# Kernel tuning notes

Measured on AMD Instinct MI355X. Metric: run time of the kernel, lower is better.

The kernel has to match this reference:

```python
import jax, jax.numpy as jnp
import numpy as np

# Mamba2 defaults: d_model=256, d_state=64, d_conv=4, expand=2, headdim=64, ngroups=1
D_MODEL = 256
NB = 2            # num_blocks
D_STATE = 64
D_CONV = 4
D_INNER = 2 * D_MODEL          # 512
HEADDIM = 64
NHEADS = D_INNER // HEADDIM    # 8
CONV_DIM = D_INNER + 2 * D_STATE           # 640
D_IN_PROJ = 2 * D_INNER + 2 * D_STATE + NHEADS  # 1160
EPS = 1e-5


def setup_inputs() -> dict:
    key = jax.random.key(0)
    ks = jax.random.split(key, 10)
    x = jax.random.normal(ks[0], (8, 32, 32, D_MODEL), dtype=jnp.float32)
    in_proj_w = jax.random.normal(ks[1], (NB, D_IN_PROJ, D_MODEL), dtype=jnp.float32) * 0.02
    conv_w = jax.random.normal(ks[2], (NB, CONV_DIM, 1, D_CONV), dtype=jnp.float32) * 0.2
    conv_b = jax.random.normal(ks[3], (NB, CONV_DIM), dtype=jnp.float32) * 0.02
    dt_bias = jax.random.normal(ks[4], (NB, NHEADS), dtype=jnp.float32) * 0.5
    # A_log = log(A), A ~ U[1,16) as in mamba2 init
    A_log = jnp.log(jax.random.uniform(ks[5], (NB, NHEADS), minval=1.0, maxval=16.0, dtype=jnp.float32))
    D = jax.random.normal(ks[6], (NB, NHEADS), dtype=jnp.float32) * 0.1 + 1.0
    norm_w = jnp.ones((NB, D_INNER), dtype=jnp.float32)
    out_proj_w = jax.random.normal(ks[7], (NB, D_MODEL, D_INNER), dtype=jnp.float32) * 0.02
    return {"x": x, "in_proj_w": in_proj_w, "conv_w": conv_w, "conv_b": conv_b,
            "dt_bias": dt_bias, "A_log": A_log, "D": D, "norm_w": norm_w,
            "out_proj_w": out_proj_w}


def _mamba2_block(h, wi, cw, cb, dtb, a_log, d_skip, nw, wo):
    B, L, _ = h.shape
    zxbcdt = jnp.einsum('blc,pc->blp', h, wi)                 # (B,L,1160)
    z = zxbcdt[..., :D_INNER]                                 # (B,L,512)
    xBC = zxbcdt[..., D_INNER:D_INNER + CONV_DIM]             # (B,L,640)
    dt = jax.nn.softplus(zxbcdt[..., -NHEADS:] + dtb)         # (B,L,8)

    # causal depthwise conv1d, kernel 4, left pad 3
    xBC = jax.lax.conv_general_dilated(
        xBC.swapaxes(1, 2), cw, window_strides=(1,), padding=[(D_CONV - 1, 0)],
        dimension_numbers=('NCH', 'OIH', 'NCH'), feature_group_count=CONV_DIM)
    xBC = jax.nn.silu((xBC + cb[None, :, None]).swapaxes(1, 2))  # (B,L,640)

    xs = xBC[..., :D_INNER].reshape(B, L, NHEADS, HEADDIM)    # (B,L,h,p)
    Bm = xBC[..., D_INNER:D_INNER + D_STATE]                  # (B,L,s) ngroups=1
    Cm = xBC[..., D_INNER + D_STATE:]                         # (B,L,s)

    A = -jnp.exp(a_log)                                       # (h,)
    dA = jnp.exp(dt * A)                                      # (B,L,h)

    def step(s, inp):
        dA_t, dt_t, x_t, B_t, C_t = inp  # (B,h),(B,h),(B,h,p),(B,s),(B,s)
        s = s * dA_t[:, :, None, None] + (dt_t[:, :, None] * x_t)[..., None] * B_t[:, None, None, :]
        y = jnp.einsum('bhps,bs->bhp', s, C_t)
        return s, y

    s0 = jnp.zeros((B, NHEADS, HEADDIM, D_STATE), dtype=h.dtype)
    _, ys = jax.lax.scan(step, s0, (dA.swapaxes(0, 1), dt.swapaxes(0, 1),
                                    xs.swapaxes(0, 1), Bm.swapaxes(0, 1), Cm.swapaxes(0, 1)))
    y = ys.swapaxes(0, 1) + d_skip[:, None] * xs              # (B,L,h,p)
    y = y.reshape(B, L, D_INNER) * jax.nn.silu(z)             # gate
    y = y * jax.lax.rsqrt(jnp.mean(y * y, axis=-1, keepdims=True) + EPS) * nw  # gated RMSNorm
    return jnp.einsum('bld,cd->blc', y, wo)


def reference(x, in_proj_w, conv_w, conv_b, dt_bias, A_log, D, norm_w, out_proj_w):
    B, H, W, C = x.shape
    h = x.reshape(B, H * W, C)
    for i in range(NB):  # stacked blocks; Dropout is identity at inference
        h = _mamba2_block(h, in_proj_w[i], conv_w[i], conv_b[i], dt_bias[i],
                          A_log[i], D[i], norm_w[i], out_proj_w[i])
    return h.reshape(B, H, W, C)
```

## Files before the change

### kernel.cpp

```cpp
#include <hip/hip_runtime.h>
#include <hip/hip_bf16.h>
#include <math.h>

#define D_MODEL   256
#define D_STATE   64
#define D_CONV    4
#define D_INNER   512
#define HEADDIM   64
#define NHEADS    8
#define CONV_DIM  640
#define D_IN_PROJ 1160
#define ZXP       1280
#define SEQLEN    1024
#define BATCH     8
#define NROWS     8192
#define EPS       1e-5f
#define CHUNK     64
#define NCHUNK    (SEQLEN / CHUNK)

typedef __attribute__((ext_vector_type(8))) short bf16x8;
typedef __attribute__((ext_vector_type(4))) short s16x4;
typedef __attribute__((ext_vector_type(8))) unsigned short u16x8;
typedef __attribute__((ext_vector_type(4))) unsigned short u16x4;
typedef __attribute__((ext_vector_type(4))) float f32x4;
typedef unsigned int u32;
typedef unsigned short u16;

__device__ __forceinline__ void cp16(const short* g, short* l) {
    __builtin_amdgcn_global_load_lds((const __attribute__((address_space(1))) u32*)g,
                                     (__attribute__((address_space(3))) u32*)l, 16, 0, 0);
}
__device__ __forceinline__ u16 bfc(float f) {
    union { __hip_bfloat16 h; u16 u; } cv;
    cv.h = __float2bfloat16(f);
    return cv.u;
}
__device__ __forceinline__ float bf2f(u16 u) {
    union { u32 v; float f; } cv;
    cv.v = ((u32)u) << 16;
    return cv.f;
}
__device__ __forceinline__ float silu_f(float a) {
    return a * __builtin_amdgcn_rcpf(1.f + __expf(-a));
}
__device__ __forceinline__ void store_out(float* p, float v) { *p = v; }
__device__ __forceinline__ void store_out(__hip_bfloat16* p, float v) { *p = __float2bfloat16(v); }

__device__ __forceinline__ int swz(int row, int col) {
    return row * 64 + (((col & 56) ^ ((row & 7) << 3)) | (col & 7));
}
__device__ __forceinline__ bf16x8 ldfrag(const short* base, int row, int oct) {
    return *(const bf16x8*)&base[row * 64 + ((oct * 8) ^ ((row & 7) * 8))];
}
__device__ __forceinline__ void wr2u(short* base, int row, int col2, u16 a, u16 b) {
    int idx = row * 64 + (((col2 & 56) ^ ((row & 7) << 3)) | (col2 & 6));
    *(u32*)&base[idx] = (u32)a | ((u32)b << 16);
}

template <typename OUT, bool WITH_DT>
__global__ __launch_bounds__(256) void gemm_mfma(const short* __restrict__ A,
                                                 const short* __restrict__ W,
                                                 OUT* __restrict__ C,
                                                 float* __restrict__ dtout,
                                                 int N, int K, int lda) {
    __shared__ short As[2 * 4096];
    __shared__ short Wsm[2 * 4096];
    const int tid  = threadIdx.x;
    const int m0   = blockIdx.y * 128;
    const int n0   = blockIdx.x * 128;
    const int wave = tid >> 6;
    const int lane = tid & 63;
    const int wm   = (wave & 1) * 64;
    const int wn   = (wave >> 1) * 64;
    const int lm   = lane & 15;
    const int lq   = lane >> 4;

    const int sr   = tid >> 2;
    const int soct = (tid & 3) ^ (sr & 3);
    const short* ga = A + (size_t)(m0 + sr) * lda + soct * 8;
    const short* gw = W + (size_t)(n0 + sr) * K + soct * 8;
    const size_t ga2 = (size_t)64 * lda;
    const size_t gw2 = (size_t)64 * K;

    const int oa = (lq ^ (lm & 3)) * 8;
    const int nt = K >> 5;

    cp16(ga,       &As[tid * 8]);
    cp16(ga + ga2, &As[2048 + tid * 8]);
    cp16(gw,       &Wsm[tid * 8]);
    cp16(gw + gw2, &Wsm[2048 + tid * 8]);
    __syncthreads();

    f32x4 acc[4][4] = {};

    for (int t = 0; t < nt; ++t) {
        const int cur = (t & 1) * 4096;
        if (t + 1 < nt) {
            const int alt = ((t + 1) & 1) * 4096;
            const short* gaN = ga + (size_t)(t + 1) * 32;
            const short* gwN = gw + (size_t)(t + 1) * 32;
            cp16(gaN,       &As[alt + tid * 8]);
            cp16(gaN + ga2, &As[alt + 2048 + tid * 8]);
            cp16(gwN,       &Wsm[alt + tid * 8]);
            cp16(gwN + gw2, &Wsm[alt + 2048 + tid * 8]);
        }
        bf16x8 af[4], bfr[4];
        #pragma unroll
        for (int i = 0; i < 4; i++) {
            af[i]  = *(const bf16x8*)&As[cur + (wm + i * 16 + lm) * 32 + oa];
            bfr[i] = *(const bf16x8*)&Wsm[cur + (wn + i * 16 + lm) * 32 + oa];
        }
        #pragma unroll
        for (int i = 0; i < 4; i++)
            #pragma unroll
            for (int j = 0; j < 4; j++)
                acc[i][j] = __builtin_amdgcn_mfma_f32_16x16x32_bf16(af[i], bfr[j], acc[i][j], 0, 0, 0);
        if (t + 1 < nt) __syncthreads();
    }
    #pragma unroll
    for (int i = 0; i < 4; i++)
        #pragma unroll
        for (int r = 0; r < 4; r++) {
            int m = m0 + wm + i * 16 + lq * 4 + r;
            #pragma unroll
            for (int j = 0; j < 4; j++) {
                int n = n0 + wn + j * 16 + lm;
                float v = acc[i][j][r];
                store_out(&C[(size_t)m * N + n], v);
                if (WITH_DT) {
                    if (n >= D_IN_PROJ - NHEADS && n < D_IN_PROJ)
                        dtout[(size_t)m * NHEADS + (n - (D_IN_PROJ - NHEADS))] = v;
                }
            }
        }
}

#define NX_C  (NROWS * D_MODEL)
#define NWI_C (2 * ZXP * D_MODEL)
#define NWO_C (2 * D_MODEL * D_INNER)
__global__ __launch_bounds__(256) void cast_all_kernel(
    const float* __restrict__ x, const float* __restrict__ wi,
    const float* __restrict__ wo,
    u16* __restrict__ xb, u16* __restrict__ wib, u16* __restrict__ wob)
{
    int idx = blockIdx.x * 256 + threadIdx.x;
    if (idx < NX_C) { xb[idx] = bfc(x[idx]); return; }
    idx -= NX_C;
    if (idx < NWI_C) {
        int k = idx & 255;
        int rb = idx >> 8;
        int r = rb % ZXP;
        int blk = rb / ZXP;
        float v = (r < D_IN_PROJ)
            ? wi[(size_t)blk * D_IN_PROJ * D_MODEL + (size_t)r * D_MODEL + k] : 0.f;
        wib[idx] = bfc(v);
        return;
    }
    idx -= NWI_C;
    wob[idx] = bfc(wo[idx]);
}

__global__ __launch_bounds__(256) void ssd_intra_kernel(
    const u16* __restrict__ zx,
    const float* __restrict__ dtbuf,
    const float* __restrict__ dt_bias, const float* __restrict__ A_log,
    const float* __restrict__ cw, const float* __restrict__ cb,
    const float* __restrict__ Dp,
    u16* __restrict__ ys, u16* __restrict__ Schunk,
    float* __restrict__ adec, u16* __restrict__ Cb)
{
    const int h   = blockIdx.x & 7;
    const int c   = (blockIdx.x >> 3) & 15;
    const int b   = blockIdx.x >> 7;
    const int tid = threadIdx.x;
    const int row0 = b * SEQLEN + c * CHUNK;

    __shared__ short Xt[64 * 64];
    __shared__ short Bn[64 * 64];
    __shared__ short Cn[64 * 64];
    __shared__ short BTw[64 * 64];
    __shared__ float cums[64], dts_s[64], ws_s[64];
    __shared__ float4 wls[192];
    __shared__ float  bls[192];

    if (tid < 64) {
        const float A = -__expf(A_log[h] * 1.44269504089f);
        float raw = dtbuf[(size_t)(row0 + tid) * NHEADS + h] + dt_bias[h];
        float dtv = (raw > 20.f) ? raw : log1pf(__expf(raw));
        float v = dtv * A;
        #pragma unroll
        for (int off = 1; off < 64; off <<= 1) {
            float o = __shfl_up(v, off, 64);
            if (tid >= off) v += o;
        }
        float tot = __shfl(v, 63, 64);
        cums[tid]  = v;
        dts_s[tid] = dtv;
        ws_s[tid]  = __expf(tot - v) * dtv;
        adec[(size_t)(b * NHEADS + h) * SEQLEN + c * CHUNK + tid] = __expf(v);
    } else {
        int wi = tid - 64;
        int g = wi >> 6, k = wi & 63;
        int ch = (g == 0) ? h * HEADDIM + k : (g == 1 ? 512 + k : 576 + k);
        wls[wi] = *(const float4*)&cw[ch * 4];
        bls[wi] = cb[ch];
    }
    __syncthreads();

    {
        const int t2 = (tid >> 3) * 2;
        const int c8 = (tid & 7) * 8;
        const int lb = c * CHUNK + t2;
        const u16* zb = zx + (size_t)(row0 + t2) * ZXP + D_INNER;
        const float w0 = ws_s[t2], w1 = ws_s[t2 + 1];
        u16x8 zz;
        #pragma unroll
        for (int q = 0; q < 8; q++) zz[q] = 0;

        #pragma unroll
        for (int g = 0; g < 3; g++) {
            const int gc = (g == 0) ? h * HEADDIM + c8 : (g == 1 ? 512 + c8 : 576 + c8);
            const u16* p = zb + gc;
            u16x8 r0 = (lb >= 3) ? *(const u16x8*)(p - 3 * ZXP) : zz;
            u16x8 r1 = (lb >= 2) ? *(const u16x8*)(p - 2 * ZXP) : zz;
            u16x8 r2 = (lb >= 1) ? *(const u16x8*)(p - 1 * ZXP) : zz;
            u16x8 r3 = *(const u16x8*)p;
            u16x8 r4 = *(const u16x8*)(p + ZXP);
            u16x8 o0, o1;
            #pragma unroll
            for (int k = 0; k < 8; k++) {
                float4 w4  = wls[g * 64 + c8 + k];
                float bias = bls[g * 64 + c8 + k];
                float a0 = bias, a1 = bias;
                a0 = fmaf(bf2f(r0[k]), w4.x, a0);
                a0 = fmaf(bf2f(r1[k]), w4.y, a0);
                a0 = fmaf(bf2f(r2[k]), w4.z, a0);
                a0 = fmaf(bf2f(r3[k]), w4.w, a0);
                a1 = fmaf(bf2f(r1[k]), w4.x, a1);
                a1 = fmaf(bf2f(r2[k]), w4.y, a1);
                a1 = fmaf(bf2f(r3[k]), w4.z, a1);
                a1 = fmaf(bf2f(r4[k]), w4.w, a1);
                float s0 = silu_f(a0);
                float s1 = silu_f(a1);
                if (g == 0) {
                    wr2u(Xt, c8 + k, t2, bfc(s0), bfc(s1));
                } else if (g == 1) {
                    o0[k] = bfc(s0); o1[k] = bfc(s1);
                    wr2u(BTw, c8 + k, t2, bfc(s0 * w0), bfc(s1 * w1));
                } else {
                    o0[k] = bfc(s0); o1[k] = bfc(s1);
                }
            }
            if (g == 1) {
                *(u16x8*)&Bn[swz(t2,     c8)] = o0;
                *(u16x8*)&Bn[swz(t2 + 1, c8)] = o1;
            } else if (g == 2) {
                *(u16x8*)&Cn[swz(t2,     c8)] = o0;
                *(u16x8*)&Cn[swz(t2 + 1, c8)] = o1;
                if (h == 0) {
                    *(u16x8*)&Cb[(size_t)(row0 + t2)     * 64 + c8] = o0;
                    *(u16x8*)&Cb[(size_t)(row0 + t2 + 1) * 64 + c8] = o1;
                }
            }
        }
    }
    __syncthreads();

    const int lane = tid & 63, w = tid >> 6;
    const int lm = lane & 15, lq = lane >> 4;
    const int tau0 = 16 * w + lq * 4;

    bf16x8 aG0 = ldfrag(Bn, 16 * w + lm, lq);
    bf16x8 aG1 = ldfrag(Bn, 16 * w + lm, 4 + lq);
    f32x4 g[4] = {};
    #pragma unroll
    for (int j = 0; j < 4; j++) {
        g[j] = __builtin_amdgcn_mfma_f32_16x16x32_bf16(aG0, ldfrag(Cn, 16 * j + lm, lq),     g[j], 0, 0, 0);
        g[j] = __builtin_amdgcn_mfma_f32_16x16x32_bf16(aG1, ldfrag(Cn, 16 * j + lm, 4 + lq), g[j], 0, 0, 0);
    }
    float ctau[4], dtau[4];
    *(float4*)&ctau[0] = *(const float4*)&cums[tau0];
    *(float4*)&dtau[0] = *(const float4*)&dts_s[tau0];
    s16x4 mp[4];
    #pragma unroll
    for (int j = 0; j < 4; j++) {
        int t = 16 * j + lm;
        float ct = cums[t];
        #pragma unroll
        for (int r = 0; r < 4; r++) {
            int tau = tau0 + r;
            float m = (t >= tau) ? g[j][r] * __expf(ct - ctau[r]) * dtau[r] : 0.f;
            mp[j][r] = (short)bfc(m);
        }
    }
    __syncthreads();
    #pragma unroll
    for (int j = 0; j < 4; j++)
        *(s16x4*)&Cn[swz(16 * j + lm, tau0)] = mp[j];
    __syncthreads();

    bf16x8 aY0 = ldfrag(Cn,  16 * w + lm, lq);
    bf16x8 aY1 = ldfrag(Cn,  16 * w + lm, 4 + lq);
    bf16x8 aS0 = ldfrag(BTw, 16 * w + lm, lq);
    bf16x8 aS1 = ldfrag(BTw, 16 * w + lm, 4 + lq);
    f32x4 yv[4] = {}, sv[4] = {};
    #pragma unroll
    for (int j = 0; j < 4; j++) {
        bf16x8 xf0 = ldfrag(Xt, 16 * j + lm, lq);
        bf16x8 xf1 = ldfrag(Xt, 16 * j + lm, 4 + lq);
        yv[j] = __builtin_amdgcn_mfma_f32_16x16x32_bf16(aY0, xf0, yv[j], 0, 0, 0);
        yv[j] = __builtin_amdgcn_mfma_f32_16x16x32_bf16(aY1, xf1, yv[j], 0, 0, 0);
        sv[j] = __builtin_amdgcn_mfma_f32_16x16x32_bf16(aS0, xf0, sv[j], 0, 0, 0);
        sv[j] = __builtin_amdgcn_mfma_f32_16x16x32_bf16(aS1, xf1, sv[j], 0, 0, 0);
    }
    const float Dh = Dp[h];
    const int mrow = 16 * w + lq * 4;
    #pragma unroll
    for (int j = 0; j < 4; j++)
        #pragma unroll
        for (int r = 0; r < 4; r++) {
            float xv = bf2f((u16)Xt[swz(16 * j + lm, mrow + r)]);
            ys[(size_t)(row0 + mrow + r) * D_INNER + h * HEADDIM + 16 * j + lm]
                = bfc(yv[j][r] + Dh * xv);
        }
    u16* sb = Schunk + (size_t)((b * NCHUNK + c) * NHEADS + h) * 4096;
    #pragma unroll
    for (int j = 0; j < 4; j++)
        #pragma unroll
        for (int r = 0; r < 4; r++)
            sb[(mrow + r) * 64 + 16 * j + lm] = bfc(sv[j][r]);
}

__global__ __launch_bounds__(256) void ssd_state_scan_kernel(
    u16* __restrict__ Schunk, const float* __restrict__ adec)
{
    const int q  = blockIdx.x & 3;
    const int bh = blockIdx.x >> 2;
    const int b  = bh >> 3, h = bh & 7;
    const int base = q * 1024 + threadIdx.x * 4;

    u16x4 v[NCHUNK];
    float atot[NCHUNK];
    #pragma unroll
    for (int c = 0; c < NCHUNK; c++) {
        v[c] = *(const u16x4*)&Schunk[(size_t)((b * NCHUNK + c) * NHEADS + h) * 4096 + base];
        atot[c] = adec[(size_t)bh * SEQLEN + c * CHUNK + 63];
    }
    float run[4] = {0.f, 0.f, 0.f, 0.f};
    #pragma unroll
    for (int c = 0; c < NCHUNK; c++) {
        u16x4 pv;
        #pragma unroll
        for (int k = 0; k < 4; k++) pv[k] = bfc(run[k]);
        *(u16x4*)&Schunk[(size_t)((b * NCHUNK + c) * NHEADS + h) * 4096 + base] = pv;
        #pragma unroll
        for (int k = 0; k < 4; k++)
            run[k] = fmaf(atot[c], run[k], bf2f(v[c][k]));
    }
}

template <typename OUT>
__global__ __launch_bounds__(512) void ssd_finish_proj_kernel(
    const u16* __restrict__ Cb, const u16* __restrict__ zx,
    const u16* __restrict__ ysin, const u16* __restrict__ Schunk,
    const float* __restrict__ adec, const float* __restrict__ nw,
    const u16* __restrict__ wo, OUT* __restrict__ Cout)
{
    const int half = blockIdx.x & 1;
    const int c    = (blockIdx.x >> 1) & 15;
    const int b    = blockIdx.x >> 5;
    const int tid  = threadIdx.x;
    const int row0 = b * SEQLEN + c * CHUNK + half * 32;

    __shared__ __align__(16) short smem[51008];
    short* y_lds = smem;
    short* Ct    = smem + 16384;
    short* STs0  = smem + 16384 + 2048;
    short* STs1  = STs0 + 4096;
    short* Ws0   = smem + 16384;
    short* Ws1   = smem + 32768;
    float* fb    = (float*)(smem + 49152);
    float* a_s   = fb;
    float* nw_s  = fb + 256;
    float* ps    = fb + 768;
    float* scl   = fb + 896;

    const int lane = tid & 63, w = tid >> 6;
    const int lm = lane & 15, lq = lane >> 4;
    const int rf  = w & 1;
    const int cf4 = w >> 1;

    nw_s[tid] = nw[tid];
    if (tid < 256) {
        int t2 = tid >> 3, n8 = (tid & 7) * 8;
        *(u16x8*)&Ct[swz(t2, n8)] = *(const u16x8*)&Cb[(size_t)(row0 + t2) * 64 + n8];
        a_s[tid] = adec[(size_t)(b * NHEADS + (tid >> 5)) * SEQLEN + c * CHUNK + half * 32 + (tid & 31)];
        const u16* sb = Schunk + (size_t)((b * NCHUNK + c) * NHEADS) * 4096;
        int n2 = (tid >> 3) * 2, p8 = (tid & 7) * 8;
        u16x8 s0 = *(const u16x8*)&sb[(size_t)n2 * 64 + p8];
        u16x8 s1 = *(const u16x8*)&sb[(size_t)(n2 + 1) * 64 + p8];
        #pragma unroll
        for (int k = 0; k < 8; k++)
            wr2u(STs0, p8 + k, n2, s0[k], s1[k]);
    }
    __syncthreads();

    bf16x8 aC0 = ldfrag(Ct, 16 * rf + lm, lq);
    bf16x8 aC1 = ldfrag(Ct, 16 * rf + lm, 4 + lq);
    float ssloc[4] = {0.f, 0.f, 0.f, 0.f};

    for (int h = 0; h < 8; h++) {
        short* Scur = (h & 1) ? STs1 : STs0;
        short* Snxt = (h & 1) ? STs0 : STs1;
        if (h < 7 && tid < 256) {
            const u16* sb = Schunk + (size_t)((b * NCHUNK + c) * NHEADS + h + 1) * 4096;
            int n2 = (tid >> 3) * 2, p8 = (tid & 7) * 8;
            u16x8 s0 = *(const u16x8*)&sb[(size_t)n2 * 64 + p8];
            u16x8 s1 = *(const u16x8*)&sb[(size_t)(n2 + 1) * 64 + p8];
            #pragma unroll
            for (int k = 0; k < 8; k++)
                wr2u(Snxt, p8 + k, n2, s0[k], s1[k]);
        }
        const int n = cf4 * 16 + lm;
        f32x4 U = {};
        U = __builtin_amdgcn_mfma_f32_16x16x32_bf16(aC0, ldfrag(Scur, n, lq),     U, 0, 0, 0);
        U = __builtin_amdgcn_mfma_f32_16x16x32_bf16(aC1, ldfrag(Scur, n, 4 + lq), U, 0, 0, 0);
        {
            const int col = h * 64 + cf4 * 16 + lm;
            const float nwv = nw_s[col];
            #pragma unroll
            for (int r = 0; r < 4; r++) {
                int row = 16 * rf + lq * 4 + r;
                size_t grow = (size_t)(row0 + row);
                float u = U[r] * a_s[h * 32 + row] + bf2f(ysin[grow * D_INNER + col]);
                float zv = bf2f(zx[grow * ZXP + col]);
                float v = u * silu_f(zv);
                ssloc[r] = fmaf(v, v, ssloc[r]);
                y_lds[row * 512 + ((((col >> 3) ^ (row & 7)) << 3) | (col & 7))] = (short)bfc(v * nwv);
            }
        }
        __syncthreads();
    }

    {
        int rr = tid >> 3, oc = tid & 7;
        #pragma unroll
        for (int q = 0; q < 4; q++) {
            int row = rr + q * 64;
            const u16* src = wo + (size_t)row * 512 + ((oc ^ (row & 7)) * 8);
            cp16((const short*)src, &Ws0[q * 4096 + tid * 8]);
        }
    }

    #pragma unroll
    for (int r = 0; r < 4; r++) {
        float s = ssloc[r];
        s += __shfl_xor(s, 1, 64); s += __shfl_xor(s, 2, 64);
        s += __shfl_xor(s, 4, 64); s += __shfl_xor(s, 8, 64);
        if (lm == 0) ps[cf4 * 32 + 16 * rf + lq * 4 + r] = s;
    }
    __syncthreads();
    if (tid < 32)
        scl[tid] = rsqrtf((ps[tid] + ps[32 + tid] + ps[64 + tid] + ps[96 + tid])
                          * (1.f / (float)D_INNER) + EPS);
    __syncthreads();

    f32x4 acc[4] = {};
    const int arow = 16 * rf + lm;
    for (int kk = 0; kk < 8; kk++) {
        short* Wcur = (kk & 1) ? Ws1 : Ws0;
        short* Wnxt = (kk & 1) ? Ws0 : Ws1;
        if (kk < 7) {
            int rr = tid >> 3, oc = tid & 7;
            #pragma unroll
            for (int q = 0; q < 4; q++) {
                int row = rr + q * 64;
                const u16* src = wo + (size_t)row * 512 + (kk + 1) * 64 + ((oc ^ (row & 7)) * 8);
                cp16((const short*)src, &Wnxt[q * 4096 + tid * 8]);
            }
        }
        bf16x8 aY0 = *(const bf16x8*)&y_lds[arow * 512 + ((kk * 8) | (lq       ^ (arow & 7))) * 8];
        bf16x8 aY1 = *(const bf16x8*)&y_lds[arow * 512 + ((kk * 8) | ((4 + lq) ^ (arow & 7))) * 8];
        #pragma unroll
        for (int j = 0; j < 4; j++) {
            int n = cf4 * 64 + j * 16 + lm;
            acc[j] = __builtin_amdgcn_mfma_f32_16x16x32_bf16(aY0, ldfrag(Wcur, n, lq),     acc[j], 0, 0, 0);
            acc[j] = __builtin_amdgcn_mfma_f32_16x16x32_bf16(aY1, ldfrag(Wcur, n, 4 + lq), acc[j], 0, 0, 0);
        }
        if (kk < 7) __syncthreads();
    }
    const int mrow = 16 * rf + lq * 4;
    #pragma unroll
    for (int r = 0; r < 4; r++) {
        float scale = scl[mrow + r];
        size_t m = (size_t)(row0 + mrow + r);
        #pragma unroll
        for (int j = 0; j < 4; j++) {
            int n = cf4 * 64 + j * 16 + lm;
            store_out(&Cout[m * D_MODEL + n], acc[j][r] * scale);
        }
    }
}

extern "C" void kernel_launch(void* const* d_in, const int* in_sizes, int n_in,
                              void* d_out, int out_size, void* d_ws, size_t ws_size,
                              hipStream_t stream) {
    const float* x          = (const float*)d_in[0];
    const float* in_proj_w  = (const float*)d_in[1];
    const float* conv_w     = (const float*)d_in[2];
    const float* conv_b     = (const float*)d_in[3];
    const float* dt_bias    = (const float*)d_in[4];
    const float* A_log      = (const float*)d_in[5];
    const float* Dp         = (const float*)d_in[6];
    const float* norm_w     = (const float*)d_in[7];
    const float* out_proj_w = (const float*)d_in[8];
    float* out = (float*)d_out;

    u16*   buf_zx = (u16*)d_ws;
    u16*   buf_cb = buf_zx + (size_t)NROWS * ZXP;
    u16*   buf_ys = buf_cb + (size_t)NROWS * 64;
    u16*   buf_S  = buf_ys + (size_t)NROWS * D_INNER;
    u16*   buf_hb = buf_S  + (size_t)BATCH * NCHUNK * NHEADS * 4096;
    u16*   buf_wi = buf_hb + (size_t)NROWS * D_MODEL;
    u16*   buf_wo = buf_wi + (size_t)2 * ZXP * D_MODEL;
    float* buf_dt = (float*)(buf_wo + (size_t)2 * D_MODEL * D_INNER);
    float* buf_a  = buf_dt + (size_t)NROWS * NHEADS;

    cast_all_kernel<<<(NX_C + NWI_C + NWO_C) / 256, 256, 0, stream>>>(
        x, in_proj_w, out_proj_w, buf_hb, buf_wi, buf_wo);

    for (int i = 0; i < 2; i++) {
        gemm_mfma<__hip_bfloat16, true><<<dim3(ZXP / 128, NROWS / 128), 256, 0, stream>>>(
            (const short*)buf_hb, (const short*)(buf_wi + (size_t)i * ZXP * D_MODEL),
            (__hip_bfloat16*)buf_zx, buf_dt, ZXP, D_MODEL, D_MODEL);

        ssd_intra_kernel<<<BATCH * NCHUNK * NHEADS, 256, 0, stream>>>(
            buf_zx, buf_dt,
            dt_bias + i * NHEADS, A_log + i * NHEADS,
            conv_w + (size_t)i * CONV_DIM * D_CONV, conv_b + (size_t)i * CONV_DIM,
            Dp + i * NHEADS, buf_ys, buf_S, buf_a, buf_cb);

        ssd_state_scan_kernel<<<BATCH * NHEADS * 4, 256, 0, stream>>>(buf_S, buf_a);

        if (i == 0) {
            ssd_finish_proj_kernel<__hip_bfloat16><<<BATCH * NCHUNK * 2, 512, 0, stream>>>(
                buf_cb, buf_zx, buf_ys, buf_S, buf_a,
                norm_w, (const u16*)buf_wo, (__hip_bfloat16*)buf_hb);
        } else {
            ssd_finish_proj_kernel<float><<<BATCH * NCHUNK * 2, 512, 0, stream>>>(
                buf_cb, buf_zx, buf_ys, buf_S, buf_a,
                norm_w + D_INNER, (const u16*)(buf_wo + (size_t)D_MODEL * D_INNER), out);
        }
    }
}
```

Measured before the change: 172.5 us.

## Remap SSD intra block order and software-prefetch ys/z loads in output kernel

Remaps the ssd_intra_kernel block index so consecutive blocks traverse chunks rather than heads, which changes locality and scheduling across the grid. In the output kernel, the per-head ys and z global loads are prefetched one head ahead into registers and the head loop is fully unrolled. The aim is to hide global load latency behind the MFMA and LDS work. The cost is higher register pressure and therefore possibly lower occupancy.

New measurement: 174.3 us. About the same (+1.1%).

```diff
diff --git a/kernel.cpp b/kernel.cpp
--- a/kernel.cpp
+++ b/kernel.cpp
@@ -169,9 +169,11 @@
     u16* __restrict__ ys, u16* __restrict__ Schunk,
     float* __restrict__ adec, u16* __restrict__ Cb)
 {
-    const int h   = blockIdx.x & 7;
-    const int c   = (blockIdx.x >> 3) & 15;
-    const int b   = blockIdx.x >> 7;
+    const int s   = blockIdx.x;
+    const int wid = (((s & 7) + ((s >> 6) << 3)) << 3) | ((s >> 3) & 7);
+    const int h   = wid & 7;
+    const int c   = (wid >> 3) & 15;
+    const int b   = wid >> 7;
     const int tid = threadIdx.x;
     const int row0 = b * SEQLEN + c * CHUNK;
 
@@ -403,15 +405,38 @@
         for (int k = 0; k < 8; k++)
             wr2u(STs0, p8 + k, n2, s0[k], s1[k]);
     }
+    float ypf[4], zpf[4];
+    {
+        const int col0 = cf4 * 16 + lm;
+        #pragma unroll
+        for (int r = 0; r < 4; r++) {
+            int row = 16 * rf + lq * 4 + r;
+            size_t grow = (size_t)(row0 + row);
+            ypf[r] = bf2f(ysin[grow * D_INNER + col0]);
+            zpf[r] = bf2f(zx[grow * ZXP + col0]);
+        }
+    }
     __syncthreads();
 
     bf16x8 aC0 = ldfrag(Ct, 16 * rf + lm, lq);
     bf16x8 aC1 = ldfrag(Ct, 16 * rf + lm, 4 + lq);
     float ssloc[4] = {0.f, 0.f, 0.f, 0.f};
 
+    #pragma unroll
     for (int h = 0; h < 8; h++) {
         short* Scur = (h & 1) ? STs1 : STs0;
         short* Snxt = (h & 1) ? STs0 : STs1;
+        float ynx[4], znx[4];
+        if (h < 7) {
+            const int coln = (h + 1) * 64 + cf4 * 16 + lm;
+            #pragma unroll
+            for (int r = 0; r < 4; r++) {
+                int row = 16 * rf + lq * 4 + r;
+                size_t grow = (size_t)(row0 + row);
+                ynx[r] = bf2f(ysin[grow * D_INNER + coln]);
+                znx[r] = bf2f(zx[grow * ZXP + coln]);
+            }
+        }
         if (h < 7 && tid < 256) {
             const u16* sb = Schunk + (size_t)((b * NCHUNK + c) * NHEADS + h + 1) * 4096;
             int n2 = (tid >> 3) * 2, p8 = (tid & 7) * 8;
@@ -431,13 +456,15 @@
             #pragma unroll
             for (int r = 0; r < 4; r++) {
                 int row = 16 * rf + lq * 4 + r;
-                size_t grow = (size_t)(row0 + row);
-                float u = U[r] * a_s[h * 32 + row] + bf2f(ysin[grow * D_INNER + col]);
-                float zv = bf2f(zx[grow * ZXP + col]);
-                float v = u * silu_f(zv);
+                float u = U[r] * a_s[h * 32 + row] + ypf[r];
+                float v = u * silu_f(zpf[r]);
                 ssloc[r] = fmaf(v, v, ssloc[r]);
                 y_lds[row * 512 + ((((col >> 3) ^ (row & 7)) << 3) | (col & 7))] = (short)bfc(v * nwv);
             }
+        }
+        if (h < 7) {
+            #pragma unroll
+            for (int r = 0; r < 4; r++) { ypf[r] = ynx[r]; zpf[r] = znx[r]; }
         }
         __syncthreads();
     }
```
